# Kernel optimization log

Hardware: AMD Instinct MI355X
Metric: run time of the kernel (lower is better)

Reference implementation:

```python
import jax, jax.numpy as jnp
import numpy as np


def setup_inputs() -> dict:
    key = jax.random.key(0)
    k1, k2 = jax.random.split(key)
    B, C, N = 8, 64, 65536
    features = jax.random.normal(k1, (B, C, N), dtype=jnp.float32)
    coords = jax.random.uniform(k2, (B, 3, N), dtype=jnp.float32)  # normalized xyz in [0,1)
    return {"features": features, "coords": coords, "resolution": 32}


def reference(features, coords, resolution):
    """avg_voxelize: quantize coords to an r^3 grid, scatter-average features.

    features: [B, C, N] float; coords: [B, 3, N] float in [0,1].
    Returns (vox [B, C, r, r, r], norm_coords [B, 3, N]).
    """
    r = resolution
    B, C, N = features.shape
    norm_coords = jnp.clip(coords * r, 0, r - 1)                 # [B, 3, N]
    vox = jnp.round(norm_coords).astype(jnp.int32)               # [B, 3, N]
    # linear voxel index per point: x*r^2 + y*r + z
    idx = (vox[:, 0] * r + vox[:, 1]) * r + vox[:, 2]            # [B, N]
    flat_idx = (idx + jnp.arange(B, dtype=jnp.int32)[:, None] * (r * r * r)).reshape(-1)  # [B*N]
    feats = features.transpose(0, 2, 1).reshape(B * N, C)        # [B*N, C]
    num_seg = B * r * r * r
    sums = jax.ops.segment_sum(feats, flat_idx, num_segments=num_seg)            # [B*r^3, C]
    cnt = jax.ops.segment_sum(jnp.ones((B * N,), features.dtype), flat_idx,
                              num_segments=num_seg)                              # [B*r^3]
    avg = sums / jnp.maximum(cnt, 1.0)[:, None]
    out = avg.reshape(B, r, r, r, C).transpose(0, 4, 1, 2, 3)    # [B, C, r, r, r]
    return out, norm_coords
```

## Files before the change

kernel.cpp:

```cpp
#include <hip/hip_runtime.h>
#include <hip/hip_bf16.h>


#define BB 8
#define CC 64
#define NN 65536
#define RR 32
#define R3 (RR * RR * RR)
#define OFFSTRIDE (R3 + 1)

__global__ __launch_bounds__(256) void points_kernel(
    const float* __restrict__ coords,
    float* __restrict__ norm_out,
    unsigned int* __restrict__ cnt,
    unsigned int* __restrict__ packed)
{
    int gid = blockIdx.x * 256 + threadIdx.x;
    int b = gid >> 16;
    int n = gid & (NN - 1);

    const float* cb = coords + (size_t)b * 3 * NN;
    float x = cb[n];
    float y = cb[NN + n];
    float z = cb[2 * NN + n];

    float nx = fminf(fmaxf(x * (float)RR, 0.0f), (float)(RR - 1));
    float ny = fminf(fmaxf(y * (float)RR, 0.0f), (float)(RR - 1));
    float nz = fminf(fmaxf(z * (float)RR, 0.0f), (float)(RR - 1));

    float* nb = norm_out + (size_t)b * 3 * NN;
    nb[n] = nx;
    nb[NN + n] = ny;
    nb[2 * NN + n] = nz;

    int vx = (int)rintf(nx);
    int vy = (int)rintf(ny);
    int vz = (int)rintf(nz);
    unsigned int idx = (unsigned int)((vx * RR + vy) * RR + vz);

    unsigned int rank = atomicAdd(&cnt[b * R3 + idx], 1u);
    packed[gid] = (idx << 17) | rank;
}

__global__ __launch_bounds__(1024) void scan_kernel(
    const unsigned int* __restrict__ cnt,
    unsigned int* __restrict__ off)
{
    int b = blockIdx.x;
    int t = threadIdx.x;
    const unsigned int* c = cnt + (size_t)b * R3;
    unsigned int* o = off + (size_t)b * OFFSTRIDE;

    unsigned int loc[32];
    unsigned int s = 0;
    #pragma unroll
    for (int k = 0; k < 32; k++) { loc[k] = c[t * 32 + k]; s += loc[k]; }

    __shared__ unsigned int aux[1024];
    aux[t] = s;
    __syncthreads();
    for (int d = 1; d < 1024; d <<= 1) {
        unsigned int v = (t >= d) ? aux[t - d] : 0u;
        __syncthreads();
        aux[t] += v;
        __syncthreads();
    }
    unsigned int run = (t == 0) ? 0u : aux[t - 1];
    #pragma unroll
    for (int k = 0; k < 32; k++) { o[t * 32 + k] = run; run += loc[k]; }
    if (t == 1023) o[R3] = run;
}

__global__ __launch_bounds__(256) void pos_kernel(
    const unsigned int* __restrict__ packed,
    const unsigned int* __restrict__ off,
    unsigned int* __restrict__ pos)
{
    int gid = blockIdx.x * 256 + threadIdx.x;
    int b = gid >> 16;
    unsigned int pk = packed[gid];
    unsigned int ix = pk >> 17;
    unsigned int rk = pk & 0x1FFFFu;
    pos[gid] = off[(size_t)b * OFFSTRIDE + ix] + rk;
}

__global__ __launch_bounds__(1024) void gather_kernel(
    const float* __restrict__ feats,
    const unsigned int* __restrict__ pos,
    const unsigned int* __restrict__ off,
    float* __restrict__ out)
{
    __shared__ __hip_bfloat16 srt[NN];

    int c = blockIdx.x;
    int b = blockIdx.y;
    int t = threadIdx.x;

    const float* f = feats + ((size_t)b * CC + c) * NN;
    const unsigned int* P = pos + (size_t)b * NN;

    for (int n0 = t * 4; n0 < NN; n0 += 1024 * 4) {
        float4 fv = *(const float4*)(f + n0);
        uint4 pv = *(const uint4*)(P + n0);
        srt[pv.x] = __float2bfloat16(fv.x);
        srt[pv.y] = __float2bfloat16(fv.y);
        srt[pv.z] = __float2bfloat16(fv.z);
        srt[pv.w] = __float2bfloat16(fv.w);
    }
    __syncthreads();

    const unsigned int* O = off + (size_t)b * OFFSTRIDE;
    float* ob = out + ((size_t)b * CC + c) * R3;
    for (int j = 0; j < 32; j++) {
        int v = t + j * 1024;
        unsigned int s0 = O[v];
        unsigned int s1 = O[v + 1];
        float s = 0.0f;
        for (unsigned int p = s0; p < s1; p++) s += __bfloat162float(srt[p]);
        float cf = (float)(s1 - s0);
        ob[v] = s / fmaxf(cf, 1.0f);
    }
}

extern "C" void kernel_launch(void* const* d_in, const int* in_sizes, int n_in,
                              void* d_out, int out_size, void* d_ws, size_t ws_size,
                              hipStream_t stream) {
    const float* feats  = (const float*)d_in[0];
    const float* coords = (const float*)d_in[1];

    float* out_vox  = (float*)d_out;
    float* out_norm = out_vox + (size_t)BB * CC * R3;

    char* ws = (char*)d_ws;
    unsigned int* cnt    = (unsigned int*)ws;
    unsigned int* off    = (unsigned int*)(ws + 1048576);
    unsigned int* packed = (unsigned int*)(ws + 1048576 + 1048608);
    unsigned int* pos    = (unsigned int*)(ws + 1048576 + 1048608 + 2097152);

    hipMemsetAsync(cnt, 0, (size_t)BB * R3 * sizeof(unsigned int), stream);

    points_kernel<<<(BB * NN) / 256, 256, 0, stream>>>(coords, out_norm, cnt, packed);
    scan_kernel<<<BB, 1024, 0, stream>>>(cnt, off);
    pos_kernel<<<(BB * NN) / 256, 256, 0, stream>>>(packed, off, pos);
    gather_kernel<<<dim3(CC, BB), 1024, 0, stream>>>(feats, pos, off, out_vox);
}
```

Before: 289.8 us.

## Sort features point-major in bf16 and reduce per voxel with padded counters

Replaces the per-channel shared-memory scatter/gather with a permute kernel that transposes features into a point-major, voxel-sorted bf16 buffer and a reduce kernel where each wave sums one voxel across 64 channels, then transposes through shared memory for coalesced output. The atomic counters are padded to 16-element stride to spread contention across cache lines. A manual bf16 rounding helper replaces the library conversion. This needs a large workspace (about 64 MB sorted buffer) and falls back to the old path if it is unavailable; it adds a global round trip of the sorted features.

```diff
diff --git a/kernel.cpp b/kernel.cpp
--- a/kernel.cpp
+++ b/kernel.cpp
@@ -1,5 +1,4 @@
 #include <hip/hip_runtime.h>
-#include <hip/hip_bf16.h>
 
 
 #define BB 8
@@ -9,11 +8,18 @@
 #define R3 (RR * RR * RR)
 #define OFFSTRIDE (R3 + 1)
 
+static __device__ inline unsigned short f2bf(float x) {
+    unsigned int u = __float_as_uint(x);
+    u += 0x7FFFu + ((u >> 16) & 1u);
+    return (unsigned short)(u >> 16);
+}
+
 __global__ __launch_bounds__(256) void points_kernel(
     const float* __restrict__ coords,
     float* __restrict__ norm_out,
     unsigned int* __restrict__ cnt,
-    unsigned int* __restrict__ packed)
+    unsigned int* __restrict__ packed,
+    int cstride)
 {
     int gid = blockIdx.x * 256 + threadIdx.x;
     int b = gid >> 16;
@@ -38,23 +44,24 @@
     int vz = (int)rintf(nz);
     unsigned int idx = (unsigned int)((vx * RR + vy) * RR + vz);
 
-    unsigned int rank = atomicAdd(&cnt[b * R3 + idx], 1u);
+    unsigned int rank = atomicAdd(&cnt[(size_t)(b * R3 + idx) * cstride], 1u);
     packed[gid] = (idx << 17) | rank;
 }
 
 __global__ __launch_bounds__(1024) void scan_kernel(
     const unsigned int* __restrict__ cnt,
-    unsigned int* __restrict__ off)
+    unsigned int* __restrict__ off,
+    int cstride)
 {
     int b = blockIdx.x;
     int t = threadIdx.x;
-    const unsigned int* c = cnt + (size_t)b * R3;
+    const unsigned int* c = cnt + (size_t)b * R3 * cstride;
     unsigned int* o = off + (size_t)b * OFFSTRIDE;
 
     unsigned int loc[32];
     unsigned int s = 0;
     #pragma unroll
-    for (int k = 0; k < 32; k++) { loc[k] = c[t * 32 + k]; s += loc[k]; }
+    for (int k = 0; k < 32; k++) { loc[k] = c[(size_t)(t * 32 + k) * cstride]; s += loc[k]; }
 
     __shared__ unsigned int aux[1024];
     aux[t] = s;
@@ -71,6 +78,91 @@
     if (t == 1023) o[R3] = run;
 }
 
+
+__global__ __launch_bounds__(256) void permute_kernel(
+    const float* __restrict__ feats,
+    const unsigned int* __restrict__ packed,
+    const unsigned int* __restrict__ off,
+    unsigned short* __restrict__ sorted)
+{
+    __shared__ float tile[64 * 65];
+    __shared__ unsigned int posb[64];
+
+    int n0 = blockIdx.x * 64;
+    int b = blockIdx.y;
+    int t = threadIdx.x;
+    const float* f = feats + (size_t)b * CC * NN;
+
+    #pragma unroll
+    for (int it = 0; it < 4; it++) {
+        int c  = (t >> 4) + 16 * it;
+        int no = (t & 15) * 4;
+        float4 fv = *(const float4*)(f + (size_t)c * NN + n0 + no);
+        tile[(no + 0) * 65 + c] = fv.x;
+        tile[(no + 1) * 65 + c] = fv.y;
+        tile[(no + 2) * 65 + c] = fv.z;
+        tile[(no + 3) * 65 + c] = fv.w;
+    }
+    if (t < 64) {
+        unsigned int pk = packed[(size_t)b * NN + n0 + t];
+        posb[t] = off[(size_t)b * OFFSTRIDE + (pk >> 17)] + (pk & 0x1FFFFu);
+    }
+    __syncthreads();
+
+    int n = t >> 2, q = t & 3;
+    unsigned int p = posb[n];
+    unsigned int w[8];
+    #pragma unroll
+    for (int k = 0; k < 8; k++) {
+        unsigned short a = f2bf(tile[n * 65 + q * 16 + 2 * k]);
+        unsigned short d = f2bf(tile[n * 65 + q * 16 + 2 * k + 1]);
+        w[k] = (unsigned int)a | ((unsigned int)d << 16);
+    }
+    unsigned short* dst = sorted + ((size_t)b * NN + p) * CC + q * 16;
+    uint4 lo = make_uint4(w[0], w[1], w[2], w[3]);
+    uint4 hi = make_uint4(w[4], w[5], w[6], w[7]);
+    *(uint4*)dst = lo;
+    *((uint4*)dst + 1) = hi;
+}
+
+__global__ __launch_bounds__(256) void reduce_kernel(
+    const unsigned short* __restrict__ sorted,
+    const unsigned int* __restrict__ off,
+    float* __restrict__ out)
+{
+    __shared__ float tile[64 * 129];
+
+    int v0 = blockIdx.x * 128;
+    int b = blockIdx.y;
+    int wave = threadIdx.x >> 6;
+    int lane = threadIdx.x & 63;
+    const unsigned int* O = off + (size_t)b * OFFSTRIDE;
+    const unsigned short* S = sorted + (size_t)b * NN * CC;
+
+    for (int w = 0; w < 32; w++) {
+        int v = v0 + wave * 32 + w;
+        unsigned int s0 = O[v];
+        unsigned int s1 = O[v + 1];
+        float s = 0.0f;
+        for (unsigned int p = s0; p < s1; p++) {
+            unsigned int u = (unsigned int)S[(size_t)p * CC + lane] << 16;
+            s += __uint_as_float(u);
+        }
+        float cf = (float)(s1 - s0);
+        tile[lane * 129 + wave * 32 + w] = s / fmaxf(cf, 1.0f);
+    }
+    __syncthreads();
+
+    float* ob = out + (size_t)b * CC * R3 + v0;
+    for (int k = 0; k < 32; k++) {
+        int id = threadIdx.x + 256 * k;
+        int c = id >> 7;
+        int dv = id & 127;
+        ob[(size_t)c * R3 + dv] = tile[c * 129 + dv];
+    }
+}
+
+
 __global__ __launch_bounds__(256) void pos_kernel(
     const unsigned int* __restrict__ packed,
     const unsigned int* __restrict__ off,
@@ -79,9 +171,7 @@
     int gid = blockIdx.x * 256 + threadIdx.x;
     int b = gid >> 16;
     unsigned int pk = packed[gid];
-    unsigned int ix = pk >> 17;
-    unsigned int rk = pk & 0x1FFFFu;
-    pos[gid] = off[(size_t)b * OFFSTRIDE + ix] + rk;
+    pos[gid] = off[(size_t)b * OFFSTRIDE + (pk >> 17)] + (pk & 0x1FFFFu);
 }
 
 __global__ __launch_bounds__(1024) void gather_kernel(
@@ -90,7 +180,7 @@
     const unsigned int* __restrict__ off,
     float* __restrict__ out)
 {
-    __shared__ __hip_bfloat16 srt[NN];
+    __shared__ unsigned short srt[NN];
 
     int c = blockIdx.x;
     int b = blockIdx.y;
@@ -102,10 +192,10 @@
     for (int n0 = t * 4; n0 < NN; n0 += 1024 * 4) {
         float4 fv = *(const float4*)(f + n0);
         uint4 pv = *(const uint4*)(P + n0);
-        srt[pv.x] = __float2bfloat16(fv.x);
-        srt[pv.y] = __float2bfloat16(fv.y);
-        srt[pv.z] = __float2bfloat16(fv.z);
-        srt[pv.w] = __float2bfloat16(fv.w);
+        srt[pv.x] = f2bf(fv.x);
+        srt[pv.y] = f2bf(fv.y);
+        srt[pv.z] = f2bf(fv.z);
+        srt[pv.w] = f2bf(fv.w);
     }
     __syncthreads();
 
@@ -116,9 +206,9 @@
         unsigned int s0 = O[v];
         unsigned int s1 = O[v + 1];
         float s = 0.0f;
-        for (unsigned int p = s0; p < s1; p++) s += __bfloat162float(srt[p]);
-        float cf = (float)(s1 - s0);
-        ob[v] = s / fmaxf(cf, 1.0f);
+        for (unsigned int p = s0; p < s1; p++)
+            s += __uint_as_float((unsigned int)srt[p] << 16);
+        ob[v] = s / fmaxf((float)(s1 - s0), 1.0f);
     }
 }
 
@@ -132,15 +222,34 @@
     float* out_norm = out_vox + (size_t)BB * CC * R3;
 
     char* ws = (char*)d_ws;
-    unsigned int* cnt    = (unsigned int*)ws;
-    unsigned int* off    = (unsigned int*)(ws + 1048576);
-    unsigned int* packed = (unsigned int*)(ws + 1048576 + 1048608);
-    unsigned int* pos    = (unsigned int*)(ws + 1048576 + 1048608 + 2097152);
-
-    hipMemsetAsync(cnt, 0, (size_t)BB * R3 * sizeof(unsigned int), stream);
-
-    points_kernel<<<(BB * NN) / 256, 256, 0, stream>>>(coords, out_norm, cnt, packed);
-    scan_kernel<<<BB, 1024, 0, stream>>>(cnt, off);
-    pos_kernel<<<(BB * NN) / 256, 256, 0, stream>>>(packed, off, pos);
-    gather_kernel<<<dim3(CC, BB), 1024, 0, stream>>>(feats, pos, off, out_vox);
-}
+
+    const size_t CNT_PAD_BYTES = (size_t)BB * R3 * 16 * 4;
+    const size_t OFF_BYTES     = (size_t)BB * OFFSTRIDE * 4;
+    const size_t PACKED_BYTES  = (size_t)BB * NN * 4;
+    const size_t SORTED_BYTES  = (size_t)BB * NN * CC * 2;
+    const size_t NEED1 = CNT_PAD_BYTES + OFF_BYTES + PACKED_BYTES + SORTED_BYTES;
+
+    if (ws_size >= NEED1) {
+        unsigned int* cnt    = (unsigned int*)ws;
+        unsigned int* off    = (unsigned int*)(ws + CNT_PAD_BYTES);
+        unsigned int* packed = (unsigned int*)(ws + CNT_PAD_BYTES + OFF_BYTES);
+        unsigned short* sorted = (unsigned short*)(ws + CNT_PAD_BYTES + OFF_BYTES + PACKED_BYTES);
+
+        hipMemsetAsync(cnt, 0, CNT_PAD_BYTES, stream);
+        points_kernel<<<(BB * NN) / 256, 256, 0, stream>>>(coords, out_norm, cnt, packed, 16);
+        scan_kernel<<<BB, 1024, 0, stream>>>(cnt, off, 16);
+        permute_kernel<<<dim3(NN / 64, BB), 256, 0, stream>>>(feats, packed, off, sorted);
+        reduce_kernel<<<dim3(R3 / 128, BB), 256, 0, stream>>>(sorted, off, out_vox);
+    } else {
+        unsigned int* cnt    = (unsigned int*)ws;
+        unsigned int* off    = (unsigned int*)(ws + 1048576);
+        unsigned int* packed = (unsigned int*)(ws + 1048576 + OFF_BYTES);
+        unsigned int* pos    = (unsigned int*)(ws + 1048576 + OFF_BYTES + PACKED_BYTES);
+
+        hipMemsetAsync(cnt, 0, 1048576, stream);
+        points_kernel<<<(BB * NN) / 256, 256, 0, stream>>>(coords, out_norm, cnt, packed, 1);
+        scan_kernel<<<BB, 1024, 0, stream>>>(cnt, off, 1);
+        pos_kernel<<<(BB * NN) / 256, 256, 0, stream>>>(packed, off, pos);
+        gather_kernel<<<dim3(CC, BB), 1024, 0, stream>>>(feats, pos, off, out_vox);
+    }
+}
```

Result: slower. 391.1 us (+35.0%).
